# Kernel optimization log

Hardware: AMD Instinct MI355X
Metric: run time of the kernel (lower is better)

## Reference

```python
import jax, jax.numpy as jnp
import numpy as np

B, C, W, H = 4, 128, 64, 64

def setup_inputs() -> dict:
    key = jax.random.key(0)
    ks = jax.random.split(key, 10)
    s = 1.0 / np.sqrt(C)
    return {
        "x": jax.random.normal(ks[0], (B, C, W, H), dtype=jnp.float32),
        "wq": jax.random.normal(ks[1], (C, C), dtype=jnp.float32) * s,
        "bq": jax.random.normal(ks[2], (C,), dtype=jnp.float32) * s,
        "wk": jax.random.normal(ks[3], (C, C), dtype=jnp.float32) * s,
        "bk": jax.random.normal(ks[4], (C,), dtype=jnp.float32) * s,
        "wv": jax.random.normal(ks[5], (C, C), dtype=jnp.float32) * s,
        "bv": jax.random.normal(ks[6], (C,), dtype=jnp.float32) * s,
        "wo": jax.random.normal(ks[7], (C, C), dtype=jnp.float32) * s,
        "bo": jax.random.normal(ks[8], (C,), dtype=jnp.float32) * s,
        "gamma": jax.random.normal(ks[9], (1,), dtype=jnp.float32),
    }

def reference(x, wq, bq, wk, bk, wv, bv, wo, bo, gamma):
    b, c, w, h = x.shape
    n = w * h
    xf = x.reshape(b, c, n)  # [B,C,N]
    # 1x1 conv == per-position matmul over channels
    q = jnp.einsum('oc,bcn->bon', wq, xf) + bq[:, None]
    k = jnp.einsum('oc,bcn->bon', wk, xf) + bk[:, None]
    v = jnp.einsum('oc,bcn->bon', wv, xf) + bv[:, None]
    # attention[b,n,m] = sum_c q[b,c,n] * k[b,c,m]
    scores = jnp.einsum('bcn,bcm->bnm', q, k) / jnp.sqrt(jnp.asarray(c, x.dtype))
    attn = jax.nn.softmax(scores, axis=-1)  # [B,N,N]
    # out[b,c,n] = sum_m v[b,c,m] * attn[b,n,m]
    out = jnp.einsum('bcm,bnm->bcn', v, attn)
    y = jnp.einsum('oc,bcn->bon', wo, out) + bo[:, None]
    y = y.reshape(b, c, w, h)
    return gamma[0] * y + x
```

## Files before the change

### kernel.cpp

```cpp
#include <hip/hip_runtime.h>

#define BN 4
#define CH 128
#define NN 4096
#define SCALE_Q 0.088388347648318447f

typedef __attribute__((ext_vector_type(8))) short s8b;
typedef __attribute__((ext_vector_type(4))) float f32x4;
typedef __attribute__((ext_vector_type(8))) unsigned short us8;
typedef __attribute__((ext_vector_type(4))) unsigned short us4;

#define MFMA16(a, b, c) __builtin_amdgcn_mfma_f32_16x16x32_bf16((a), (b), (c), 0, 0, 0)

#define GLOAD16(gsrc, ldst) __builtin_amdgcn_global_load_lds( \
    (const __attribute__((address_space(1))) unsigned int*)(gsrc), \
    (__attribute__((address_space(3))) unsigned int*)(ldst), 16, 0, 0)

__device__ __forceinline__ unsigned short f2bf(float f) {
  union { float f; unsigned int u; } v; v.f = f;
  unsigned int r = v.u + 0x7fffu + ((v.u >> 16) & 1u);
  return (unsigned short)(r >> 16);
}
__device__ __forceinline__ float bf2f(unsigned short h) {
  union { unsigned int u; float f; } v; v.u = (unsigned int)h << 16;
  return v.f;
}

__global__ __launch_bounds__(256) void transpose_x(
    const float* __restrict__ x, unsigned short* __restrict__ Xth,
    unsigned short* __restrict__ Xtl)
{
  __shared__ unsigned short Lh[64 * 128];
  __shared__ unsigned short Ll[64 * 128];
  const int b = blockIdx.y;
  const int n0 = blockIdx.x * 64;
  const float* Xb = x + (size_t)b * CH * NN;
  const int tid = threadIdx.x;

#pragma unroll
  for (int it = 0; it < 8; ++it) {
    int idx = it * 256 + tid;
    int c = idx >> 4;
    int n4 = (idx & 15) * 4;
    float4 v = *reinterpret_cast<const float4*>(&Xb[(size_t)c * NN + n0 + n4]);
    float vv[4] = {v.x, v.y, v.z, v.w};
#pragma unroll
    for (int k = 0; k < 4; ++k) {
      int n = n4 + k;
      unsigned short hh = f2bf(vv[k]);
      unsigned short ll = f2bf(vv[k] - bf2f(hh));
      int ad = n * 128 + (c ^ ((n & 7) << 3));
      Lh[ad] = hh;
      Ll[ad] = ll;
    }
  }
  __syncthreads();
#pragma unroll
  for (int it = 0; it < 4; ++it) {
    int idx = it * 256 + tid;
    int n = idx >> 4;
    int j = idx & 15;
    int ad = n * 128 + ((j * 8) ^ ((n & 7) << 3));
    us8 h8 = *reinterpret_cast<const us8*>(&Lh[ad]);
    us8 l8 = *reinterpret_cast<const us8*>(&Ll[ad]);
    size_t go = ((size_t)b * NN + n0 + n) * CH + j * 8;
    *reinterpret_cast<us8*>(&Xth[go]) = h8;
    *reinterpret_cast<us8*>(&Xtl[go]) = l8;
  }
}

__global__ __launch_bounds__(256, 3) void qkv_mfma(
    const unsigned short* __restrict__ Xth, const unsigned short* __restrict__ Xtl,
    const float* __restrict__ wq, const float* __restrict__ bq,
    const float* __restrict__ wk, const float* __restrict__ bk,
    const float* __restrict__ wv, const float* __restrict__ bv,
    unsigned short* __restrict__ Qt, unsigned short* __restrict__ Kt,
    unsigned short* __restrict__ Vn)
{
  __shared__ __align__(16) unsigned short Xh[64 * 128];
  __shared__ __align__(16) unsigned short Xl[64 * 128];

  const int b = blockIdx.y;
  const int n0 = blockIdx.x * 64;
  const int z = blockIdx.z;
  const float* W; const float* bias;
  if (z == 0)      { W = wq; bias = bq; }
  else if (z == 1) { W = wk; bias = bk; }
  else             { W = wv; bias = bv; }

  const int tid = threadIdx.x;
  const int w = tid >> 6, lane = tid & 63, l15 = lane & 15, g = lane >> 4;
  const int ob = w * 32;

  const unsigned short* XhB = Xth + ((size_t)b * NN + n0) * CH;
  const unsigned short* XlB = Xtl + ((size_t)b * NN + n0) * CH;
#pragma unroll
  for (int i = 0; i < 4; ++i) {
    int base = i * 4096 + w * 1024;
    int loff = base + lane * 16;
    int row = loff >> 8;
    int chunk = (loff >> 4) & 15;
    int sk = chunk ^ (row & 7);
    GLOAD16(XhB + (size_t)row * CH + sk * 8, ((unsigned char*)Xh) + base);
    GLOAD16(XlB + (size_t)row * CH + sk * 8, ((unsigned char*)Xl) + base);
  }

  s8b ah[2][4], al[2][4];
#pragma unroll
  for (int m = 0; m < 2; ++m)
#pragma unroll
    for (int kk = 0; kk < 4; ++kk) {
      int o = ob + m * 16 + l15;
      int c = (kk * 4 + g) * 8;
      float4 w0 = *reinterpret_cast<const float4*>(&W[o * CH + c]);
      float4 w1 = *reinterpret_cast<const float4*>(&W[o * CH + c + 4]);
      float wv8[8] = {w0.x, w0.y, w0.z, w0.w, w1.x, w1.y, w1.z, w1.w};
      s8b hh, ll;
#pragma unroll
      for (int t = 0; t < 8; ++t) {
        unsigned short hv = f2bf(wv8[t]);
        hh[t] = (short)hv;
        ll[t] = (short)f2bf(wv8[t] - bf2f(hv));
      }
      ah[m][kk] = hh;
      al[m][kk] = ll;
    }
  __syncthreads();

  f32x4 acc[2][4];
#pragma unroll
  for (int m = 0; m < 2; ++m)
#pragma unroll
    for (int nst = 0; nst < 4; ++nst)
#pragma unroll
      for (int r = 0; r < 4; ++r) acc[m][nst][r] = 0.f;

#pragma unroll
  for (int kk = 0; kk < 4; ++kk)
#pragma unroll
    for (int nst = 0; nst < 4; ++nst) {
      int n = nst * 16 + l15;
      int ck = (kk * 4 + g) ^ (n & 7);
      s8b bh = *reinterpret_cast<const s8b*>(&Xh[n * 128 + ck * 8]);
      s8b bl = *reinterpret_cast<const s8b*>(&Xl[n * 128 + ck * 8]);
#pragma unroll
      for (int m = 0; m < 2; ++m) {
        acc[m][nst] = MFMA16(ah[m][kk], bh, acc[m][nst]);
        acc[m][nst] = MFMA16(ah[m][kk], bl, acc[m][nst]);
        acc[m][nst] = MFMA16(al[m][kk], bh, acc[m][nst]);
      }
    }
  __syncthreads();

  if (z < 2) {
    const float s = (z == 0) ? SCALE_Q : 1.f;
#pragma unroll
    for (int m = 0; m < 2; ++m) {
      float4 b4 = *reinterpret_cast<const float4*>(&bias[ob + m * 16 + g * 4]);
      float bb[4] = {b4.x, b4.y, b4.z, b4.w};
#pragma unroll
      for (int nst = 0; nst < 4; ++nst) {
        int n = nst * 16 + l15;
        int slot = w * 8 + m * 4 + g;
        int sl = slot ^ (n & 7);
        us4 pk;
#pragma unroll
        for (int r = 0; r < 4; ++r) pk[r] = f2bf((acc[m][nst][r] + bb[r]) * s);
        *reinterpret_cast<us4*>(&Xh[n * 128 + sl * 4]) = pk;
      }
    }
    __syncthreads();
    unsigned short* T = (z == 0 ? Qt : Kt) + ((size_t)b * NN + n0) * CH;
#pragma unroll
    for (int it = 0; it < 4; ++it) {
      int idx = it * 256 + tid;
      int n = idx >> 4;
      int j = idx & 15;
      int s0 = (2 * j) ^ (n & 7);
      int s1 = (2 * j + 1) ^ (n & 7);
      us4 a4 = *reinterpret_cast<const us4*>(&Xh[n * 128 + s0 * 4]);
      us4 b4 = *reinterpret_cast<const us4*>(&Xh[n * 128 + s1 * 4]);
      us8 o8;
#pragma unroll
      for (int t = 0; t < 4; ++t) { o8[t] = a4[t]; o8[4 + t] = b4[t]; }
      *reinterpret_cast<us8*>(&T[n * CH + j * 8]) = o8;
    }
  } else {
#pragma unroll
    for (int m = 0; m < 2; ++m) {
      float4 b4 = *reinterpret_cast<const float4*>(&bias[ob + m * 16 + g * 4]);
      float bb[4] = {b4.x, b4.y, b4.z, b4.w};
#pragma unroll
      for (int nst = 0; nst < 4; ++nst) {
        int n = nst * 16 + l15;
#pragma unroll
        for (int r = 0; r < 4; ++r) {
          int o = ob + m * 16 + g * 4 + r;
          Xh[o * 64 + (n ^ ((o & 7) << 3))] = f2bf(acc[m][nst][r] + bb[r]);
        }
      }
    }
    __syncthreads();
    unsigned short* V = Vn + (size_t)b * CH * NN;
#pragma unroll
    for (int it = 0; it < 4; ++it) {
      int idx = it * 256 + tid;
      int o = idx >> 3;
      int j8 = idx & 7;
      us8 v8 = *reinterpret_cast<const us8*>(&Xh[o * 64 + ((j8 ^ (o & 7)) << 3)]);
      *reinterpret_cast<us8*>(&V[(size_t)o * NN + n0 + j8 * 8]) = v8;
    }
  }
}

#define FLASH_STAGE(BI, KT) do {                                            \
    int m0_ = (KT) * 128;                                                   \
    _Pragma("unroll")                                                       \
    for (int i_ = 0; i_ < 4; ++i_) {                                        \
      int base_ = i_ * 8192 + w * 1024;                                     \
      int loff_ = base_ + lane * 16;                                        \
      int row_ = loff_ >> 8;                                                \
      int chunk_ = (loff_ >> 4) & 15;                                       \
      int sk_ = chunk_ ^ (row_ & 7);                                        \
      GLOAD16(Kb + (size_t)(m0_ + row_) * CH + sk_ * 8,                     \
              smem + (BI) * 32768 + base_);                                 \
      GLOAD16(Vb + (size_t)row_ * NN + m0_ + sk_ * 8,                       \
              smem + 65536 + (BI) * 32768 + base_);                         \
    }                                                                       \
  } while (0)

__global__ __launch_bounds__(512, 2) void flash_attn_mfma(
    const unsigned short* __restrict__ Qt,
    const unsigned short* __restrict__ Kt,
    const unsigned short* __restrict__ Vn,
    unsigned short* __restrict__ Oth, unsigned short* __restrict__ Otl)
{
  __shared__ __align__(16) unsigned char smem[147456];

  const int flat = blockIdx.y * 64 + blockIdx.x;
  const int swz = (flat & 7) * 32 + (flat >> 3);
  const int b = swz >> 6;
  const int n0 = (swz & 63) * 64;

  const int tid = threadIdx.x;
  const int w = tid >> 6, lane = tid & 63, l15 = lane & 15, g = lane >> 4;
  const int rhalf = w & 1;
  const int h = w >> 1;

  const unsigned short* Qb = Qt + (size_t)b * NN * CH;
  const unsigned short* Kb = Kt + (size_t)b * NN * CH;
  const unsigned short* Vb = Vn + (size_t)b * CH * NN;

  s8b qf[2][4];
#pragma unroll
  for (int m = 0; m < 2; ++m)
#pragma unroll
    for (int kk = 0; kk < 4; ++kk) {
      int row = n0 + rhalf * 32 + m * 16 + l15;
      int c = (kk * 4 + g) * 8;
      qf[m][kk] = *reinterpret_cast<const s8b*>(&Qb[(size_t)row * CH + c]);
    }

  f32x4 facc[2][8];
#pragma unroll
  for (int m = 0; m < 2; ++m)
#pragma unroll
    for (int cst = 0; cst < 8; ++cst)
#pragma unroll
      for (int r = 0; r < 4; ++r) facc[m][cst][r] = 0.f;
  float m_run[2][4], l_run[2][4];
#pragma unroll
  for (int m = 0; m < 2; ++m)
#pragma unroll
    for (int r = 0; r < 4; ++r) { m_run[m][r] = -1e30f; l_run[m][r] = 0.f; }

  FLASH_STAGE(0, 0);
  __syncthreads();

  int cur = 0;
  for (int kt = 0; kt < 32; ++kt) {
    if (kt + 1 < 32) FLASH_STAGE(cur ^ 1, kt + 1);
    const unsigned short* Ks = (const unsigned short*)(smem + cur * 32768);
    const unsigned short* Vs = (const unsigned short*)(smem + 65536 + cur * 32768);
    unsigned short* Pw = (unsigned short*)(smem + 131072 + w * 2048);

    f32x4 sacc[2][2];
#pragma unroll
    for (int m = 0; m < 2; ++m)
#pragma unroll
      for (int st = 0; st < 2; ++st)
#pragma unroll
        for (int r = 0; r < 4; ++r) sacc[m][st][r] = 0.f;
#pragma unroll
    for (int kk = 0; kk < 4; ++kk)
#pragma unroll
      for (int st = 0; st < 2; ++st) {
        int key = h * 32 + st * 16 + l15;
        int ck = (kk * 4 + g) ^ (key & 7);
        s8b bf = *reinterpret_cast<const s8b*>(&Ks[key * 128 + ck * 8]);
        sacc[0][st] = MFMA16(qf[0][kk], bf, sacc[0][st]);
        sacc[1][st] = MFMA16(qf[1][kk], bf, sacc[1][st]);
      }

#pragma unroll
    for (int m = 0; m < 2; ++m)
#pragma unroll
      for (int r = 0; r < 4; ++r) {
        float s0 = sacc[m][0][r], s1 = sacc[m][1][r];
        float t = fmaxf(s0, s1);
        t = fmaxf(t, __shfl_xor(t, 1));
        t = fmaxf(t, __shfl_xor(t, 2));
        t = fmaxf(t, __shfl_xor(t, 4));
        t = fmaxf(t, __shfl_xor(t, 8));
        float mn = fmaxf(m_run[m][r], t);
        float f = __expf(m_run[m][r] - mn);
        float p0 = __expf(s0 - mn), p1 = __expf(s1 - mn);
        float rs = p0 + p1;
        rs += __shfl_xor(rs, 1);
        rs += __shfl_xor(rs, 2);
        rs += __shfl_xor(rs, 4);
        rs += __shfl_xor(rs, 8);
        l_run[m][r] = l_run[m][r] * f + rs;
        m_run[m][r] = mn;
#pragma unroll
        for (int cst = 0; cst < 8; ++cst) facc[m][cst][r] *= f;
        int rw = m * 16 + g * 4 + r;
        int k0 = l15, k1 = 16 + l15;
        Pw[rw * 32 + (((k0 >> 3) ^ (rw & 3)) << 3) + (k0 & 7)] = f2bf(p0);
        Pw[rw * 32 + (((k1 >> 3) ^ (rw & 3)) << 3) + (k1 & 7)] = f2bf(p1);
      }

    s8b pa[2];
#pragma unroll
    for (int m = 0; m < 2; ++m) {
      int rw = m * 16 + l15;
      int kc = g ^ (rw & 3);
      pa[m] = *reinterpret_cast<const s8b*>(&Pw[rw * 32 + (kc << 3)]);
    }
#pragma unroll
    for (int cst = 0; cst < 8; ++cst) {
      int c = cst * 16 + l15;
      int ck = (h * 4 + g) ^ (c & 7);
      s8b vf = *reinterpret_cast<const s8b*>(&Vs[c * 128 + ck * 8]);
      facc[0][cst] = MFMA16(pa[0], vf, facc[0][cst]);
      facc[1][cst] = MFMA16(pa[1], vf, facc[1][cst]);
    }
    __syncthreads();
    cur ^= 1;
  }

  float* Mb = (float*)smem;
  float* Lb = (float*)(smem + 1024);
  float* Db = (float*)(smem + 2048);
  float* Obuf = (float*)(smem + 4096);

  if (l15 == 0) {
#pragma unroll
    for (int m = 0; m < 2; ++m)
#pragma unroll
      for (int r = 0; r < 4; ++r) {
        int ra = rhalf * 32 + m * 16 + g * 4 + r;
        Mb[h * 64 + ra] = m_run[m][r];
        Lb[h * 64 + ra] = l_run[m][r];
      }
  }
  __syncthreads();
  float fsc[2][4];
#pragma unroll
  for (int m = 0; m < 2; ++m)
#pragma unroll
    for (int r = 0; r < 4; ++r) {
      int ra = rhalf * 32 + m * 16 + g * 4 + r;
      float M = fmaxf(fmaxf(Mb[ra], Mb[64 + ra]), fmaxf(Mb[128 + ra], Mb[192 + ra]));
      fsc[m][r] = __expf(m_run[m][r] - M);
      if (h == 0 && l15 == 0) {
        float den = Lb[ra] * __expf(Mb[ra] - M) + Lb[64 + ra] * __expf(Mb[64 + ra] - M) +
                    Lb[128 + ra] * __expf(Mb[128 + ra] - M) +
                    Lb[192 + ra] * __expf(Mb[192 + ra] - M);
        Db[ra] = 1.f / den;
      }
    }
  __syncthreads();
#pragma unroll
  for (int t = 0; t < 4; ++t) {
    if (h == t) {
#pragma unroll
      for (int m = 0; m < 2; ++m)
#pragma unroll
        for (int cst = 0; cst < 8; ++cst)
#pragma unroll
          for (int r = 0; r < 4; ++r) {
            int ra = rhalf * 32 + m * 16 + g * 4 + r;
            int c = cst * 16 + l15;
            float v = facc[m][cst][r] * fsc[m][r];
            if (t == 0) Obuf[ra * 132 + c] = v;
            else        Obuf[ra * 132 + c] += v;
          }
    }
    __syncthreads();
  }
#pragma unroll
  for (int it = 0; it < 2; ++it) {
    int idx = it * 512 + tid;
    int row = idx >> 4;
    int j = idx & 15;
    float inv = Db[row];
    us8 hh, ll;
#pragma unroll
    for (int t = 0; t < 8; ++t) {
      float v = Obuf[row * 132 + j * 8 + t] * inv;
      unsigned short hv = f2bf(v);
      hh[t] = hv;
      ll[t] = f2bf(v - bf2f(hv));
    }
    size_t go = ((size_t)b * NN + n0 + row) * CH + j * 8;
    *reinterpret_cast<us8*>(&Oth[go]) = hh;
    *reinterpret_cast<us8*>(&Otl[go]) = ll;
  }
}

__global__ __launch_bounds__(256, 2) void out_mfma(
    const unsigned short* __restrict__ Oth, const unsigned short* __restrict__ Otl,
    const float* __restrict__ wo, const float* __restrict__ bo,
    const float* __restrict__ x, const float* __restrict__ gamma,
    float* __restrict__ y)
{
  __shared__ __align__(16) unsigned char smem[67584];
  unsigned short* Oh = (unsigned short*)smem;
  unsigned short* Ol = (unsigned short*)(smem + 16384);
  float* Obuf = (float*)(smem + 32768);

  const int b = blockIdx.y;
  const int n0 = blockIdx.x * 64;
  const int tid = threadIdx.x;
  const int w = tid >> 6, lane = tid & 63, l15 = lane & 15, g = lane >> 4;
  const int ob = w * 32;

  const unsigned short* OhB = Oth + ((size_t)b * NN + n0) * CH;
  const unsigned short* OlB = Otl + ((size_t)b * NN + n0) * CH;
#pragma unroll
  for (int i = 0; i < 4; ++i) {
    int base = i * 4096 + w * 1024;
    int loff = base + lane * 16;
    int row = loff >> 8;
    int chunk = (loff >> 4) & 15;
    int sk = chunk ^ (row & 7);
    GLOAD16(OhB + (size_t)row * CH + sk * 8, smem + base);
    GLOAD16(OlB + (size_t)row * CH + sk * 8, smem + 16384 + base);
  }

  s8b ah[2][4], al[2][4];
#pragma unroll
  for (int m = 0; m < 2; ++m)
#pragma unroll
    for (int kk = 0; kk < 4; ++kk) {
      int o = ob + m * 16 + l15;
      int c = (kk * 4 + g) * 8;
      float4 w0 = *reinterpret_cast<const float4*>(&wo[o * CH + c]);
      float4 w1 = *reinterpret_cast<const float4*>(&wo[o * CH + c + 4]);
      float wv8[8] = {w0.x, w0.y, w0.z, w0.w, w1.x, w1.y, w1.z, w1.w};
      s8b hh, ll;
#pragma unroll
      for (int t = 0; t < 8; ++t) {
        unsigned short hv = f2bf(wv8[t]);
        hh[t] = (short)hv;
        ll[t] = (short)f2bf(wv8[t] - bf2f(hv));
      }
      ah[m][kk] = hh;
      al[m][kk] = ll;
    }
  const float gm = gamma[0];
  __syncthreads();

  f32x4 acc[2][4];
#pragma unroll
  for (int m = 0; m < 2; ++m)
#pragma unroll
    for (int nst = 0; nst < 4; ++nst)
#pragma unroll
      for (int r = 0; r < 4; ++r) acc[m][nst][r] = 0.f;

#pragma unroll
  for (int kk = 0; kk < 4; ++kk)
#pragma unroll
    for (int nst = 0; nst < 4; ++nst) {
      int n = nst * 16 + l15;
      int ck = (kk * 4 + g) ^ (n & 7);
      s8b bh = *reinterpret_cast<const s8b*>(&Oh[n * 128 + ck * 8]);
      s8b bl = *reinterpret_cast<const s8b*>(&Ol[n * 128 + ck * 8]);
#pragma unroll
      for (int m = 0; m < 2; ++m) {
        acc[m][nst] = MFMA16(ah[m][kk], bh, acc[m][nst]);
        acc[m][nst] = MFMA16(ah[m][kk], bl, acc[m][nst]);
        acc[m][nst] = MFMA16(al[m][kk], bh, acc[m][nst]);
      }
    }
  __syncthreads();

#pragma unroll
  for (int m = 0; m < 2; ++m) {
    float4 b4 = *reinterpret_cast<const float4*>(&bo[ob + m * 16 + g * 4]);
    float bb[4] = {b4.x, b4.y, b4.z, b4.w};
#pragma unroll
    for (int nst = 0; nst < 4; ++nst) {
      int n = nst * 16 + l15;
#pragma unroll
      for (int r = 0; r < 4; ++r) {
        int o = ob + m * 16 + g * 4 + r;
        Obuf[o * 68 + n] = gm * (acc[m][nst][r] + bb[r]);
      }
    }
  }
  __syncthreads();
  const float* Xb = x + (size_t)b * CH * NN;
  float* Yb = y + (size_t)b * CH * NN;
#pragma unroll
  for (int it = 0; it < 8; ++it) {
    int idx = it * 256 + tid;
    int o = idx >> 4;
    int n4 = (idx & 15) * 4;
    float4 v = *reinterpret_cast<const float4*>(&Obuf[o * 68 + n4]);
    float4 rx = *reinterpret_cast<const float4*>(&Xb[(size_t)o * NN + n0 + n4]);
    v.x += rx.x; v.y += rx.y; v.z += rx.z; v.w += rx.w;
    *reinterpret_cast<float4*>(&Yb[(size_t)o * NN + n0 + n4]) = v;
  }
}

extern "C" void kernel_launch(void* const* d_in, const int* in_sizes, int n_in,
                              void* d_out, int out_size, void* d_ws, size_t ws_size,
                              hipStream_t stream) {
  const float* x     = (const float*)d_in[0];
  const float* wq    = (const float*)d_in[1];
  const float* bq    = (const float*)d_in[2];
  const float* wk    = (const float*)d_in[3];
  const float* bk    = (const float*)d_in[4];
  const float* wv    = (const float*)d_in[5];
  const float* bv    = (const float*)d_in[6];
  const float* wo    = (const float*)d_in[7];
  const float* bo    = (const float*)d_in[8];
  const float* gamma = (const float*)d_in[9];
  float* y = (float*)d_out;

  const size_t per = (size_t)BN * NN * CH;
  unsigned short* Xth = (unsigned short*)d_ws;
  unsigned short* Xtl = Xth + per;
  unsigned short* Qt  = Xtl + per;
  unsigned short* Kt  = Qt + per;
  unsigned short* Vn  = Kt + per;
  unsigned short* Oth = Vn + per;
  unsigned short* Otl = Oth + per;

  transpose_x<<<dim3(NN / 64, BN), 256, 0, stream>>>(x, Xth, Xtl);
  qkv_mfma<<<dim3(NN / 64, BN, 3), 256, 0, stream>>>(Xth, Xtl, wq, bq, wk, bk,
                                                     wv, bv, Qt, Kt, Vn);
  flash_attn_mfma<<<dim3(64, BN), 512, 0, stream>>>(Qt, Kt, Vn, Oth, Otl);
  out_mfma<<<dim3(NN / 64, BN), 256, 0, stream>>>(Oth, Otl, wo, bo, x, gamma, y);
}
```

Measured before the change: 202.0 us.

## Fuse x transpose into QKV and rework flash attention with exp2 and lazy rescale

Removes the separate transpose kernel: the QKV kernel now reads fp32 x directly and splits it into bf16 hi/lo in shared memory. Flash attention is restructured to 256-thread blocks of 32 query rows, using single-buffered K/V loads with two barriers per tile instead of the double-buffered pipeline. Q is prescaled by log2(e)/sqrt(C) so exp2 can replace exp. The running max is only updated when it grows by more than 8, and the row-sum reduction is deferred to the end. Wave priority hints wrap the MFMA sections. Dropping the double buffering exposes load latency, and the lazy rescale lets unnormalised probabilities grow up to 2^8, which reduces precision margin.

```diff
diff --git a/kernel.cpp b/kernel.cpp
--- a/kernel.cpp
+++ b/kernel.cpp
@@ -3,7 +3,7 @@
 #define BN 4
 #define CH 128
 #define NN 4096
-#define SCALE_Q 0.088388347648318447f
+#define SCALE_QL2 0.12751744954339238f
 
 typedef __attribute__((ext_vector_type(8))) short s8b;
 typedef __attribute__((ext_vector_type(4))) float f32x4;
@@ -26,51 +26,8 @@
   return v.f;
 }
 
-__global__ __launch_bounds__(256) void transpose_x(
-    const float* __restrict__ x, unsigned short* __restrict__ Xth,
-    unsigned short* __restrict__ Xtl)
-{
-  __shared__ unsigned short Lh[64 * 128];
-  __shared__ unsigned short Ll[64 * 128];
-  const int b = blockIdx.y;
-  const int n0 = blockIdx.x * 64;
-  const float* Xb = x + (size_t)b * CH * NN;
-  const int tid = threadIdx.x;
-
-#pragma unroll
-  for (int it = 0; it < 8; ++it) {
-    int idx = it * 256 + tid;
-    int c = idx >> 4;
-    int n4 = (idx & 15) * 4;
-    float4 v = *reinterpret_cast<const float4*>(&Xb[(size_t)c * NN + n0 + n4]);
-    float vv[4] = {v.x, v.y, v.z, v.w};
-#pragma unroll
-    for (int k = 0; k < 4; ++k) {
-      int n = n4 + k;
-      unsigned short hh = f2bf(vv[k]);
-      unsigned short ll = f2bf(vv[k] - bf2f(hh));
-      int ad = n * 128 + (c ^ ((n & 7) << 3));
-      Lh[ad] = hh;
-      Ll[ad] = ll;
-    }
-  }
-  __syncthreads();
-#pragma unroll
-  for (int it = 0; it < 4; ++it) {
-    int idx = it * 256 + tid;
-    int n = idx >> 4;
-    int j = idx & 15;
-    int ad = n * 128 + ((j * 8) ^ ((n & 7) << 3));
-    us8 h8 = *reinterpret_cast<const us8*>(&Lh[ad]);
-    us8 l8 = *reinterpret_cast<const us8*>(&Ll[ad]);
-    size_t go = ((size_t)b * NN + n0 + n) * CH + j * 8;
-    *reinterpret_cast<us8*>(&Xth[go]) = h8;
-    *reinterpret_cast<us8*>(&Xtl[go]) = l8;
-  }
-}
-
-__global__ __launch_bounds__(256, 3) void qkv_mfma(
-    const unsigned short* __restrict__ Xth, const unsigned short* __restrict__ Xtl,
+__global__ __launch_bounds__(256, 2) void qkv_fused(
+    const float* __restrict__ x,
     const float* __restrict__ wq, const float* __restrict__ bq,
     const float* __restrict__ wk, const float* __restrict__ bk,
     const float* __restrict__ wv, const float* __restrict__ bv,
@@ -87,22 +44,28 @@
   if (z == 0)      { W = wq; bias = bq; }
   else if (z == 1) { W = wk; bias = bk; }
   else             { W = wv; bias = bv; }
+  const float* Xb = x + (size_t)b * CH * NN;
 
   const int tid = threadIdx.x;
   const int w = tid >> 6, lane = tid & 63, l15 = lane & 15, g = lane >> 4;
   const int ob = w * 32;
 
-  const unsigned short* XhB = Xth + ((size_t)b * NN + n0) * CH;
-  const unsigned short* XlB = Xtl + ((size_t)b * NN + n0) * CH;
-#pragma unroll
-  for (int i = 0; i < 4; ++i) {
-    int base = i * 4096 + w * 1024;
-    int loff = base + lane * 16;
-    int row = loff >> 8;
-    int chunk = (loff >> 4) & 15;
-    int sk = chunk ^ (row & 7);
-    GLOAD16(XhB + (size_t)row * CH + sk * 8, ((unsigned char*)Xh) + base);
-    GLOAD16(XlB + (size_t)row * CH + sk * 8, ((unsigned char*)Xl) + base);
+#pragma unroll
+  for (int it = 0; it < 8; ++it) {
+    int idx = it * 256 + tid;
+    int c = idx >> 4;
+    int n4 = (idx & 15) * 4;
+    float4 v = *reinterpret_cast<const float4*>(&Xb[(size_t)c * NN + n0 + n4]);
+    float vv[4] = {v.x, v.y, v.z, v.w};
+#pragma unroll
+    for (int k = 0; k < 4; ++k) {
+      int n = n4 + k;
+      unsigned short hh = f2bf(vv[k]);
+      unsigned short ll = f2bf(vv[k] - bf2f(hh));
+      int ad = n * 128 + (c ^ ((n & 7) << 3));
+      Xh[ad] = hh;
+      Xl[ad] = ll;
+    }
   }
 
   s8b ah[2][4], al[2][4];
@@ -153,7 +116,7 @@
   __syncthreads();
 
   if (z < 2) {
-    const float s = (z == 0) ? SCALE_Q : 1.f;
+    const float s = (z == 0) ? SCALE_QL2 : 1.f;
 #pragma unroll
     for (int m = 0; m < 2; ++m) {
       float4 b4 = *reinterpret_cast<const float4*>(&bias[ob + m * 16 + g * 4]);
@@ -213,39 +176,21 @@
   }
 }
 
-#define FLASH_STAGE(BI, KT) do {                                            \
-    int m0_ = (KT) * 128;                                                   \
-    _Pragma("unroll")                                                       \
-    for (int i_ = 0; i_ < 4; ++i_) {                                        \
-      int base_ = i_ * 8192 + w * 1024;                                     \
-      int loff_ = base_ + lane * 16;                                        \
-      int row_ = loff_ >> 8;                                                \
-      int chunk_ = (loff_ >> 4) & 15;                                       \
-      int sk_ = chunk_ ^ (row_ & 7);                                        \
-      GLOAD16(Kb + (size_t)(m0_ + row_) * CH + sk_ * 8,                     \
-              smem + (BI) * 32768 + base_);                                 \
-      GLOAD16(Vb + (size_t)row_ * NN + m0_ + sk_ * 8,                       \
-              smem + 65536 + (BI) * 32768 + base_);                         \
-    }                                                                       \
-  } while (0)
-
-__global__ __launch_bounds__(512, 2) void flash_attn_mfma(
+__global__ __launch_bounds__(256, 2) void flash_attn_v4(
     const unsigned short* __restrict__ Qt,
     const unsigned short* __restrict__ Kt,
     const unsigned short* __restrict__ Vn,
     unsigned short* __restrict__ Oth, unsigned short* __restrict__ Otl)
 {
-  __shared__ __align__(16) unsigned char smem[147456];
-
-  const int flat = blockIdx.y * 64 + blockIdx.x;
-  const int swz = (flat & 7) * 32 + (flat >> 3);
-  const int b = swz >> 6;
-  const int n0 = (swz & 63) * 64;
+  __shared__ __align__(16) unsigned char smem[73728];
+
+  const int flat = blockIdx.y * 128 + blockIdx.x;
+  const int swz = (flat & 7) * 64 + (flat >> 3);
+  const int b = swz >> 7;
+  const int n0 = (swz & 127) * 32;
 
   const int tid = threadIdx.x;
   const int w = tid >> 6, lane = tid & 63, l15 = lane & 15, g = lane >> 4;
-  const int rhalf = w & 1;
-  const int h = w >> 1;
 
   const unsigned short* Qb = Qt + (size_t)b * NN * CH;
   const unsigned short* Kb = Kt + (size_t)b * NN * CH;
@@ -256,7 +201,7 @@
   for (int m = 0; m < 2; ++m)
 #pragma unroll
     for (int kk = 0; kk < 4; ++kk) {
-      int row = n0 + rhalf * 32 + m * 16 + l15;
+      int row = n0 + m * 16 + l15;
       int c = (kk * 4 + g) * 8;
       qf[m][kk] = *reinterpret_cast<const s8b*>(&Qb[(size_t)row * CH + c]);
     }
@@ -274,15 +219,23 @@
 #pragma unroll
     for (int r = 0; r < 4; ++r) { m_run[m][r] = -1e30f; l_run[m][r] = 0.f; }
 
-  FLASH_STAGE(0, 0);
-  __syncthreads();
-
-  int cur = 0;
+  const unsigned short* Ks = (const unsigned short*)smem;
+  const unsigned short* Vs = (const unsigned short*)(smem + 32768);
+  unsigned short* Pw = (unsigned short*)(smem + 65536) + w * 1024;
+
   for (int kt = 0; kt < 32; ++kt) {
-    if (kt + 1 < 32) FLASH_STAGE(cur ^ 1, kt + 1);
-    const unsigned short* Ks = (const unsigned short*)(smem + cur * 32768);
-    const unsigned short* Vs = (const unsigned short*)(smem + 65536 + cur * 32768);
-    unsigned short* Pw = (unsigned short*)(smem + 131072 + w * 2048);
+    const int m0 = kt * 128;
+    __syncthreads();
+#pragma unroll
+    for (int i = 0; i < 8; ++i) {
+      int loff = i * 4096 + tid * 16;
+      int row = loff >> 8;
+      int chunk = (loff >> 4) & 15;
+      int sk = chunk ^ (row & 7);
+      GLOAD16(Kb + (size_t)(m0 + row) * CH + sk * 8, smem + loff);
+      GLOAD16(Vb + (size_t)row * NN + m0 + sk * 8, smem + 32768 + loff);
+    }
+    __syncthreads();
 
     f32x4 sacc[2][2];
 #pragma unroll
@@ -291,124 +244,143 @@
       for (int st = 0; st < 2; ++st)
 #pragma unroll
         for (int r = 0; r < 4; ++r) sacc[m][st][r] = 0.f;
+    __builtin_amdgcn_s_setprio(1);
 #pragma unroll
     for (int kk = 0; kk < 4; ++kk)
 #pragma unroll
       for (int st = 0; st < 2; ++st) {
-        int key = h * 32 + st * 16 + l15;
+        int key = w * 32 + st * 16 + l15;
         int ck = (kk * 4 + g) ^ (key & 7);
         s8b bf = *reinterpret_cast<const s8b*>(&Ks[key * 128 + ck * 8]);
         sacc[0][st] = MFMA16(qf[0][kk], bf, sacc[0][st]);
         sacc[1][st] = MFMA16(qf[1][kk], bf, sacc[1][st]);
       }
+    __builtin_amdgcn_s_setprio(0);
 
 #pragma unroll
     for (int m = 0; m < 2; ++m)
 #pragma unroll
       for (int r = 0; r < 4; ++r) {
         float s0 = sacc[m][0][r], s1 = sacc[m][1][r];
-        float t = fmaxf(s0, s1);
-        t = fmaxf(t, __shfl_xor(t, 1));
-        t = fmaxf(t, __shfl_xor(t, 2));
-        t = fmaxf(t, __shfl_xor(t, 4));
-        t = fmaxf(t, __shfl_xor(t, 8));
-        float mn = fmaxf(m_run[m][r], t);
-        float f = __expf(m_run[m][r] - mn);
-        float p0 = __expf(s0 - mn), p1 = __expf(s1 - mn);
-        float rs = p0 + p1;
-        rs += __shfl_xor(rs, 1);
-        rs += __shfl_xor(rs, 2);
-        rs += __shfl_xor(rs, 4);
-        rs += __shfl_xor(rs, 8);
-        l_run[m][r] = l_run[m][r] * f + rs;
-        m_run[m][r] = mn;
-#pragma unroll
-        for (int cst = 0; cst < 8; ++cst) facc[m][cst][r] *= f;
+        float mt = fmaxf(s0, s1);
+        mt = fmaxf(mt, __shfl_xor(mt, 1));
+        mt = fmaxf(mt, __shfl_xor(mt, 2));
+        mt = fmaxf(mt, __shfl_xor(mt, 4));
+        mt = fmaxf(mt, __shfl_xor(mt, 8));
+        if (__any(mt > m_run[m][r] + 8.f)) {
+          float mn = fmaxf(m_run[m][r], mt);
+          float f = exp2f(m_run[m][r] - mn);
+          l_run[m][r] *= f;
+#pragma unroll
+          for (int cst = 0; cst < 8; ++cst) facc[m][cst][r] *= f;
+          m_run[m][r] = mn;
+        }
+        float p0 = exp2f(s0 - m_run[m][r]);
+        float p1 = exp2f(s1 - m_run[m][r]);
+        l_run[m][r] += p0 + p1;
         int rw = m * 16 + g * 4 + r;
-        int k0 = l15, k1 = 16 + l15;
-        Pw[rw * 32 + (((k0 >> 3) ^ (rw & 3)) << 3) + (k0 & 7)] = f2bf(p0);
-        Pw[rw * 32 + (((k1 >> 3) ^ (rw & 3)) << 3) + (k1 & 7)] = f2bf(p1);
+        int sch0 = (l15 >> 3) ^ g;
+        int sch1 = (2 + (l15 >> 3)) ^ g;
+        Pw[rw * 32 + sch0 * 8 + (l15 & 7)] = f2bf(p0);
+        Pw[rw * 32 + sch1 * 8 + (l15 & 7)] = f2bf(p1);
       }
 
     s8b pa[2];
 #pragma unroll
     for (int m = 0; m < 2; ++m) {
-      int rw = m * 16 + l15;
-      int kc = g ^ (rw & 3);
-      pa[m] = *reinterpret_cast<const s8b*>(&Pw[rw * 32 + (kc << 3)]);
-    }
+      int row = m * 16 + l15;
+      int sch = g ^ (l15 >> 2);
+      pa[m] = *reinterpret_cast<const s8b*>(&Pw[row * 32 + sch * 8]);
+    }
+    __builtin_amdgcn_s_setprio(1);
 #pragma unroll
     for (int cst = 0; cst < 8; ++cst) {
       int c = cst * 16 + l15;
-      int ck = (h * 4 + g) ^ (c & 7);
+      int ck = (w * 4 + g) ^ (c & 7);
       s8b vf = *reinterpret_cast<const s8b*>(&Vs[c * 128 + ck * 8]);
       facc[0][cst] = MFMA16(pa[0], vf, facc[0][cst]);
       facc[1][cst] = MFMA16(pa[1], vf, facc[1][cst]);
     }
+    __builtin_amdgcn_s_setprio(0);
+  }
+
+  float l_red[2][4];
+#pragma unroll
+  for (int m = 0; m < 2; ++m)
+#pragma unroll
+    for (int r = 0; r < 4; ++r) {
+      float rs = l_run[m][r];
+      rs += __shfl_xor(rs, 1);
+      rs += __shfl_xor(rs, 2);
+      rs += __shfl_xor(rs, 4);
+      rs += __shfl_xor(rs, 8);
+      l_red[m][r] = rs;
+    }
+  __syncthreads();
+
+  float* Mb = (float*)smem;
+  float* Lb = (float*)(smem + 512);
+  float* Db = (float*)(smem + 1024);
+  float* Obuf = (float*)(smem + 2048);
+
+  if (l15 == 0) {
+#pragma unroll
+    for (int m = 0; m < 2; ++m)
+#pragma unroll
+      for (int r = 0; r < 4; ++r) {
+        int ra = m * 16 + g * 4 + r;
+        Mb[w * 32 + ra] = m_run[m][r];
+        Lb[w * 32 + ra] = l_red[m][r];
+      }
+  }
+  __syncthreads();
+  float fsc[2][4];
+#pragma unroll
+  for (int m = 0; m < 2; ++m)
+#pragma unroll
+    for (int r = 0; r < 4; ++r) {
+      int ra = m * 16 + g * 4 + r;
+      float M = fmaxf(fmaxf(Mb[ra], Mb[32 + ra]), fmaxf(Mb[64 + ra], Mb[96 + ra]));
+      fsc[m][r] = exp2f(m_run[m][r] - M);
+      if (w == 0 && l15 == 0) {
+        float den = Lb[ra] * exp2f(Mb[ra] - M) + Lb[32 + ra] * exp2f(Mb[32 + ra] - M) +
+                    Lb[64 + ra] * exp2f(Mb[64 + ra] - M) +
+                    Lb[96 + ra] * exp2f(Mb[96 + ra] - M);
+        Db[ra] = 1.f / den;
+      }
+    }
+#pragma unroll
+  for (int t = 0; t < 4; ++t) {
     __syncthreads();
-    cur ^= 1;
-  }
-
-  float* Mb = (float*)smem;
-  float* Lb = (float*)(smem + 1024);
-  float* Db = (float*)(smem + 2048);
-  float* Obuf = (float*)(smem + 4096);
-
-  if (l15 == 0) {
-#pragma unroll
-    for (int m = 0; m < 2; ++m)
-#pragma unroll
-      for (int r = 0; r < 4; ++r) {
-        int ra = rhalf * 32 + m * 16 + g * 4 + r;
-        Mb[h * 64 + ra] = m_run[m][r];
-        Lb[h * 64 + ra] = l_run[m][r];
-      }
-  }
-  __syncthreads();
-  float fsc[2][4];
-#pragma unroll
-  for (int m = 0; m < 2; ++m)
-#pragma unroll
-    for (int r = 0; r < 4; ++r) {
-      int ra = rhalf * 32 + m * 16 + g * 4 + r;
-      float M = fmaxf(fmaxf(Mb[ra], Mb[64 + ra]), fmaxf(Mb[128 + ra], Mb[192 + ra]));
-      fsc[m][r] = __expf(m_run[m][r] - M);
-      if (h == 0 && l15 == 0) {
-        float den = Lb[ra] * __expf(Mb[ra] - M) + Lb[64 + ra] * __expf(Mb[64 + ra] - M) +
-                    Lb[128 + ra] * __expf(Mb[128 + ra] - M) +
-                    Lb[192 + ra] * __expf(Mb[192 + ra] - M);
-        Db[ra] = 1.f / den;
-      }
-    }
-  __syncthreads();
-#pragma unroll
-  for (int t = 0; t < 4; ++t) {
-    if (h == t) {
+    if (w == t) {
 #pragma unroll
       for (int m = 0; m < 2; ++m)
 #pragma unroll
         for (int cst = 0; cst < 8; ++cst)
 #pragma unroll
           for (int r = 0; r < 4; ++r) {
-            int ra = rhalf * 32 + m * 16 + g * 4 + r;
+            int ra = m * 16 + g * 4 + r;
             int c = cst * 16 + l15;
             float v = facc[m][cst][r] * fsc[m][r];
             if (t == 0) Obuf[ra * 132 + c] = v;
             else        Obuf[ra * 132 + c] += v;
           }
     }
-    __syncthreads();
-  }
+  }
+  __syncthreads();
 #pragma unroll
   for (int it = 0; it < 2; ++it) {
-    int idx = it * 512 + tid;
+    int idx = it * 256 + tid;
     int row = idx >> 4;
     int j = idx & 15;
     float inv = Db[row];
+    float4 v0 = *reinterpret_cast<const float4*>(&Obuf[row * 132 + j * 8]);
+    float4 v1 = *reinterpret_cast<const float4*>(&Obuf[row * 132 + j * 8 + 4]);
+    float vv[8] = {v0.x, v0.y, v0.z, v0.w, v1.x, v1.y, v1.z, v1.w};
     us8 hh, ll;
 #pragma unroll
     for (int t = 0; t < 8; ++t) {
-      float v = Obuf[row * 132 + j * 8 + t] * inv;
+      float v = vv[t] * inv;
       unsigned short hv = f2bf(v);
       hh[t] = hv;
       ll[t] = f2bf(v - bf2f(hv));
@@ -542,17 +514,14 @@
   float* y = (float*)d_out;
 
   const size_t per = (size_t)BN * NN * CH;
-  unsigned short* Xth = (unsigned short*)d_ws;
-  unsigned short* Xtl = Xth + per;
-  unsigned short* Qt  = Xtl + per;
+  unsigned short* Qt  = (unsigned short*)d_ws;
   unsigned short* Kt  = Qt + per;
   unsigned short* Vn  = Kt + per;
   unsigned short* Oth = Vn + per;
   unsigned short* Otl = Oth + per;
 
-  transpose_x<<<dim3(NN / 64, BN), 256, 0, stream>>>(x, Xth, Xtl);
-  qkv_mfma<<<dim3(NN / 64, BN, 3), 256, 0, stream>>>(Xth, Xtl, wq, bq, wk, bk,
-                                                     wv, bv, Qt, Kt, Vn);
-  flash_attn_mfma<<<dim3(64, BN), 512, 0, stream>>>(Qt, Kt, Vn, Oth, Otl);
+  qkv_fused<<<dim3(NN / 64, BN, 3), 256, 0, stream>>>(x, wq, bq, wk, bk, wv, bv,
+                                                      Qt, Kt, Vn);
+  flash_attn_v4<<<dim3(NN / 32, BN), 256, 0, stream>>>(Qt, Kt, Vn, Oth, Otl);
   out_mfma<<<dim3(NN / 64, BN), 256, 0, stream>>>(Oth, Otl, wo, bo, x, gamma, y);
 }
```

New measurement: 204.3 us. Within noise of the previous version (+1.1%).
